# Optimization experiments

Measured on AMD Instinct MI355X. Metric: run time of the kernel, lower is better.

The kernel has to match this reference:

```python
import jax, jax.numpy as jnp
import numpy as np

N_NODES = 10000
N_EDGES = 320000


def _segment_softmax(scores, seg, num_segments):
    # scores: [E, H], segment-wise stable softmax keyed by seg (edge_index[0])
    m = jax.ops.segment_max(scores, seg, num_segments=num_segments)
    e = jnp.exp(scores - m[seg])
    z = jax.ops.segment_sum(e, seg, num_segments=num_segments)
    return e / z[seg]


def _gat_layer(x, W, a, row, col, n_nodes, heads, out_dim):
    # x: [N, F_in], W: [F_in, heads*out_dim], a: [heads, 2*out_dim]
    h = (x @ W).reshape(n_nodes, heads, out_dim)          # [N, H, F]
    a_l, a_r = a[:, :out_dim], a[:, out_dim:]             # [H, F] each
    # attention score per edge/head without materializing [E, H, 2F]
    s = (h[row] * a_l).sum(-1) + (h[col] * a_r).sum(-1)   # [E, H]
    alpha = _segment_softmax(s, row, n_nodes)             # [E, H]
    msg = alpha[..., None] * h[row]                       # [E, H, F]
    return jax.ops.segment_sum(msg, col, num_segments=n_nodes)  # [N, H, F]


def setup_inputs() -> dict:
    key = jax.random.key(0)
    ks = jax.random.split(key, 6)
    F, H, C = 128, 4, 22
    x = jax.random.normal(ks[0], (N_NODES, F), dtype=jnp.float32)
    edge_index = jax.random.randint(ks[1], (2, N_EDGES), 0, N_NODES, dtype=jnp.int64)
    W1 = jax.random.normal(ks[2], (F, F * H), dtype=jnp.float32) * 0.05
    a1 = jax.random.normal(ks[3], (H, 2 * F), dtype=jnp.float32) * 0.05
    W2 = jax.random.normal(ks[4], (F, C), dtype=jnp.float32) * 0.05
    a2 = jax.random.normal(ks[5], (1, 2 * C), dtype=jnp.float32) * 0.05
    return {"x": x, "edge_index": edge_index, "W1": W1, "a1": a1, "W2": W2, "a2": a2}


def reference(x, edge_index, W1, a1, W2, a2):
    row, col = edge_index[0], edge_index[1]
    h1 = _gat_layer(x, W1, a1, row, col, N_NODES, heads=4, out_dim=128)  # [N, 4, 128]
    h1 = jax.nn.elu(h1).mean(axis=1)                                      # combine heads -> [N, 128]
    h2 = _gat_layer(h1, W2, a2, row, col, N_NODES, heads=1, out_dim=22)   # [N, 1, 22]
    return h2[:, 0, :]                                                    # [N, 22]
```

## Files before the change

kernel.cpp:

```cpp
#include <hip/hip_runtime.h>

#define NN 10000
#define NE 320000
#define EPP 5000
#define NPART 64

typedef short short8 __attribute__((ext_vector_type(8)));
typedef float f32x4 __attribute__((ext_vector_type(4)));

__device__ __forceinline__ unsigned short f2bf(float f) {
    unsigned u = __float_as_uint(f);
    return (unsigned short)((u + 0x7FFFu + ((u >> 16) & 1u)) >> 16);
}
__device__ __forceinline__ float bflo(unsigned v) { return __uint_as_float(v << 16); }
__device__ __forceinline__ float bfhi(unsigned v) { return __uint_as_float(v & 0xffff0000u); }
__device__ __forceinline__ float bf1(unsigned short v) { return __uint_as_float(((unsigned)v) << 16); }

__device__ __forceinline__ int eread(const void* p, int is64, int i) {
    if (is64) return (int)((const long long*)p)[i];
    return ((const int*)p)[i];
}

__global__ __launch_bounds__(256) void k_prep0(const void* __restrict__ ei,
                                               const float* __restrict__ W1, const float* __restrict__ a1,
                                               unsigned short* __restrict__ W1t, float* __restrict__ wrf,
                                               int* __restrict__ flag) {
    const int b = blockIdx.x, t = threadIdx.x;
    if (b < 256) {
        const int g = b * 256 + t;
        const int h = g >> 14, j = (g >> 7) & 127, k = g & 127;
        W1t[g] = f2bf(W1[(size_t)k * 512 + h * 128 + j]);
    } else if (b < 258) {
        const int g = (b - 256) * 256 + t;
        const int h = g >> 7, k = g & 127;
        const float* wrow = W1 + (size_t)k * 512 + h * 128;
        const float* av = a1 + h * 256 + 128;
        float s = 0.f;
        for (int d = 0; d < 128; d++) s += wrow[d] * av[d];
        wrf[h * 128 + k] = s;
    } else {
        if (t == 0) {
            const unsigned* idx = (const unsigned*)ei;
            int all0 = 1;
            for (int j = 1; j < 257; j += 2)
                if (idx[j] != 0u) { all0 = 0; break; }
            *flag = all0;
        }
    }
}

__global__ __launch_bounds__(256) void k_pre(const float* __restrict__ x, const float* __restrict__ wrf,
                                             unsigned short* __restrict__ xb, float* __restrict__ ehr1,
                                             const void* __restrict__ ei, const int* __restrict__ flag,
                                             unsigned short* __restrict__ degp_c,
                                             unsigned short* __restrict__ degp_r,
                                             unsigned* __restrict__ packed_c,
                                             unsigned* __restrict__ packed_r) {
    __shared__ int sh[NN];
    const int b = blockIdx.x, t = threadIdx.x;
    if (b < 2500) {
        float* ls = (float*)sh;
        const int lane = t & 63, w = t >> 6;
        ls[t] = wrf[t];
        ls[t + 256] = wrf[t + 256];
        __syncthreads();
        const int i = b * 4 + w;
        const float x0 = x[(size_t)i * 128 + lane];
        const float x1 = x[(size_t)i * 128 + 64 + lane];
        xb[(size_t)i * 128 + lane]      = f2bf(x0);
        xb[(size_t)i * 128 + 64 + lane] = f2bf(x1);
        float v[4];
#pragma unroll
        for (int h = 0; h < 4; h++)
            v[h] = x0 * ls[h * 128 + lane] + x1 * ls[h * 128 + 64 + lane];
#pragma unroll
        for (int off = 1; off < 64; off <<= 1) {
#pragma unroll
            for (int j = 0; j < 4; j++) v[j] += __shfl_xor(v[j], off);
        }
        if (lane == 0)
            *(float4*)&ehr1[i * 4] = make_float4(__expf(v[0]), __expf(v[1]), __expf(v[2]), __expf(v[3]));
    } else {
        const int is64 = *flag;
        const int isC = (b < 2500 + NPART);
        const int p = isC ? (b - 2500) : (b - 2500 - NPART);
        const int ebase = p * EPP;
        for (int q = t; q < NN; q += 256) sh[q] = 0;
        __syncthreads();
        if (isC) {
            for (int q = t; q < EPP; q += 256) {
                const int e = ebase + q;
                const int c = eread(ei, is64, NE + e);
                const unsigned rk = (unsigned)atomicAdd(&sh[c], 1);
                packed_c[e] = ((unsigned)c << 13) | rk;
            }
            __syncthreads();
            for (int q = t; q < NN; q += 256) degp_c[p * NN + q] = (unsigned short)sh[q];
        } else {
            for (int q = t; q < EPP; q += 256) {
                const int e = ebase + q;
                const int r = eread(ei, is64, e);
                const unsigned rk = (unsigned)atomicAdd(&sh[r], 1);
                packed_r[e] = ((unsigned)r << 13) | rk;
            }
            __syncthreads();
            for (int q = t; q < NN; q += 256) degp_r[p * NN + q] = (unsigned short)sh[q];
        }
    }
}

__global__ __launch_bounds__(256) void k_psum(const unsigned short* __restrict__ degp_c,
                                              const unsigned short* __restrict__ degp_r,
                                              unsigned short* __restrict__ pfx_c,
                                              unsigned short* __restrict__ pfx_r,
                                              int* __restrict__ deg_c, int* __restrict__ deg_r) {
    const int g = blockIdx.x * 256 + threadIdx.x;
    if (g >= 2 * NN) return;
    const int arr = g / NN, node = g % NN;
    const unsigned short* degp = arr ? degp_r : degp_c;
    unsigned short* pfx = arr ? pfx_r : pfx_c;
    int* tot = arr ? deg_r : deg_c;
    int sum = 0;
#pragma unroll
    for (int p = 0; p < NPART; p++) {
        pfx[p * NN + node] = (unsigned short)sum;
        sum += (int)degp[p * NN + node];
    }
    tot[node] = sum;
}

__device__ void scan_one_1k(const int* __restrict__ deg, int* __restrict__ start, int* ssum) {
    const int t = threadIdx.x;
    int loc[10];
    const int base = t * 10;
    int sum = 0;
#pragma unroll
    for (int j = 0; j < 10; j++) {
        int i = base + j;
        int v = (i < NN) ? deg[i] : 0;
        loc[j] = sum;
        sum += v;
    }
    const int lane = t & 63, w = t >> 6;
    int xi = sum;
#pragma unroll
    for (int off = 1; off < 64; off <<= 1) {
        int y = __shfl_up(xi, off);
        if (lane >= off) xi += y;
    }
    __syncthreads();
    if (lane == 63) ssum[w] = xi;
    __syncthreads();
    int woff = 0;
#pragma unroll
    for (int k = 0; k < 16; k++)
        if (k < w) woff += ssum[k];
    const int excl = woff + xi - sum;
#pragma unroll
    for (int j = 0; j < 10; j++) {
        int i = base + j;
        if (i < NN) start[i] = excl + loc[j];
    }
}

__global__ __launch_bounds__(1024) void k_scan2(const int* __restrict__ deg_c, const int* __restrict__ deg_r,
                                                int* __restrict__ start_c, int* __restrict__ start_r) {
    __shared__ int ssum[16];
    scan_one_1k(deg_c, start_c, ssum);
    __syncthreads();
    scan_one_1k(deg_r, start_r, ssum);
}

__global__ __launch_bounds__(256) void k_build(const unsigned* __restrict__ packed_c,
                                               const unsigned* __restrict__ packed_r,
                                               const unsigned short* __restrict__ pfx_c,
                                               const unsigned short* __restrict__ pfx_r,
                                               const int* __restrict__ start_c, const int* __restrict__ start_r,
                                               int* __restrict__ csrA, int* __restrict__ csrB) {
    const int e = blockIdx.x * 256 + threadIdx.x;
    if (e >= NE) return;
    const int part = e / EPP;
    const unsigned pc = packed_c[e], pr = packed_r[e];
    const int c = (int)(pc >> 13), rkc = (int)(pc & 8191u);
    const int r = (int)(pr >> 13), rkr = (int)(pr & 8191u);
    csrA[start_c[c] + (int)pfx_c[part * NN + c] + rkc] = r;
    csrB[start_r[r] + (int)pfx_r[part * NN + r] + rkr] = c;
}

__global__ __launch_bounds__(256) void k_z1(const int* __restrict__ start_r, const int* __restrict__ deg_r,
                                            const int* __restrict__ csrB,
                                            const float* __restrict__ ehr1, float* __restrict__ rz1) {
    const int t = threadIdx.x, lane = t & 63, w = t >> 6;
    const int half = lane >> 5, l32 = lane & 31;
    const int i = blockIdx.x * 8 + w * 2 + half;
    const int s0 = start_r[i], d = deg_r[i];
    float zx = 0.f, zy = 0.f, zz = 0.f, zw = 0.f;
    for (int p = s0 + l32; p < s0 + d; p += 32) {
        const int c = csrB[p];
        const float4 v = *(const float4*)&ehr1[c * 4];
        zx += v.x; zy += v.y; zz += v.z; zw += v.w;
    }
#pragma unroll
    for (int off = 1; off < 32; off <<= 1) {
        zx += __shfl_xor(zx, off); zy += __shfl_xor(zy, off);
        zz += __shfl_xor(zz, off); zw += __shfl_xor(zw, off);
    }
    if (l32 == 0)
        *(float4*)&rz1[i * 4] = make_float4(1.f / zx, 1.f / zy, 1.f / zz, 1.f / zw);
}

__global__ __launch_bounds__(1024) void k_aggF(const unsigned short* __restrict__ xb,
                                               const float* __restrict__ ehr1, const float* __restrict__ rz1,
                                               const int* __restrict__ start_c, const int* __restrict__ deg_c,
                                               const int* __restrict__ csrA,
                                               const unsigned short* __restrict__ W1t,
                                               float* __restrict__ h1m) {
    __shared__ unsigned short lx[16 * 512];
    const int t = threadIdx.x, lane = t & 63, w = t >> 6;
    const int n0 = blockIdx.x * 16;

    {
        const int i = n0 + w;
        const float4 er4 = *(const float4*)&ehr1[i * 4];
        const int s0 = start_c[i], dg = deg_c[i];
        float acc[8];
#pragma unroll
        for (int j = 0; j < 8; j++) acc[j] = 0.f;
        int p = s0;
        const int e8 = s0 + (dg & ~7);
        for (; p < e8; p += 8) {
            int rr[8]; unsigned vv[8]; float4 zz[8];
#pragma unroll
            for (int q = 0; q < 8; q++) rr[q] = csrA[p + q];
#pragma unroll
            for (int q = 0; q < 8; q++) vv[q] = *(const unsigned*)&xb[(size_t)rr[q] * 128 + lane * 2];
#pragma unroll
            for (int q = 0; q < 8; q++) zz[q] = *(const float4*)&rz1[rr[q] * 4];
#pragma unroll
            for (int q = 0; q < 8; q++) {
                const float xa = bflo(vv[q]), xbv = bfhi(vv[q]);
                acc[0] += zz[q].x * xa; acc[1] += zz[q].x * xbv;
                acc[2] += zz[q].y * xa; acc[3] += zz[q].y * xbv;
                acc[4] += zz[q].z * xa; acc[5] += zz[q].z * xbv;
                acc[6] += zz[q].w * xa; acc[7] += zz[q].w * xbv;
            }
        }
        for (; p < s0 + dg; ++p) {
            const int r = csrA[p];
            const unsigned v = *(const unsigned*)&xb[(size_t)r * 128 + lane * 2];
            const float4 z = *(const float4*)&rz1[r * 4];
            const float xa = bflo(v), xbv = bfhi(v);
            acc[0] += z.x * xa; acc[1] += z.x * xbv;
            acc[2] += z.y * xa; acc[3] += z.y * xbv;
            acc[4] += z.z * xa; acc[5] += z.z * xbv;
            acc[6] += z.w * xa; acc[7] += z.w * xbv;
        }
        const float ef[4] = {er4.x, er4.y, er4.z, er4.w};
        const int fin = (lane & 3) * 2;
#pragma unroll
        for (int h = 0; h < 4; h++) {
            const int f = h * 16 + (lane >> 2);
            const int sc = ((f ^ (w & 7)) << 3) + fin;
            ushort2 st;
            st.x = f2bf(acc[h * 2] * ef[h]);
            st.y = f2bf(acc[h * 2 + 1] * ef[h]);
            *(ushort2*)&lx[w * 512 + sc] = st;
        }
    }
    __syncthreads();

    if (w < 8) {
        const int j = w;
        const int r16 = lane & 15, grp = lane >> 4;
        f32x4 hm = (f32x4)0.f;
#pragma unroll
        for (int h = 0; h < 4; h++) {
            f32x4 acc = (f32x4)0.f;
#pragma unroll
            for (int kk = 0; kk < 128; kk += 32) {
                const int f = h * 16 + (kk >> 3) + grp;
                const int sc = (f ^ (r16 & 7)) << 3;
                short8 a = *(const short8*)&lx[r16 * 512 + sc];
                short8 bfr = *(const short8*)&W1t[(size_t)h * 16384 + (j * 16 + r16) * 128 + kk + grp * 8];
                acc = __builtin_amdgcn_mfma_f32_16x16x32_bf16(a, bfr, acc, 0, 0, 0);
            }
#pragma unroll
            for (int r = 0; r < 4; r++) {
                const float v = acc[r];
                hm[r] += (v > 0.f) ? v : (__expf(v) - 1.f);
            }
        }
#pragma unroll
        for (int r = 0; r < 4; r++) {
            const int node = n0 + grp * 4 + r;
            h1m[(size_t)node * 128 + j * 16 + r16] = 0.25f * hm[r];
        }
    }
}

__global__ __launch_bounds__(256) void k_gemm2(const float* __restrict__ h1m, const float* __restrict__ W2,
                                               const float* __restrict__ a2,
                                               float* __restrict__ h2, float* __restrict__ ehr2) {
    __shared__ float sh[4][128];
    const int t = threadIdx.x, lane = t & 63, w = t >> 6;
    const int i = blockIdx.x * 4 + w;
    sh[w][lane]      = h1m[(size_t)i * 128 + lane];
    sh[w][lane + 64] = h1m[(size_t)i * 128 + 64 + lane];
    __syncthreads();
    const int seg = lane >> 5, c = lane & 31;
    float part = 0.f;
    if (c < 22) {
        const int kb = seg * 64;
        for (int k = kb; k < kb + 64; k++)
            part += sh[w][k] * W2[k * 22 + c];
    }
    part += __shfl_xor(part, 32);
    const float acc = part;
    if (lane < 22) h2[(size_t)i * 22 + lane] = acc;
    float pr = (lane < 22) ? acc * a2[22 + lane] : 0.f;
#pragma unroll
    for (int off = 1; off < 64; off <<= 1)
        pr += __shfl_xor(pr, off);
    if (lane == 0) ehr2[i] = __expf(pr);
}

__global__ __launch_bounds__(256) void k_z2s(const int* __restrict__ start_r, const int* __restrict__ deg_r,
                                             const int* __restrict__ csrB,
                                             const float* __restrict__ ehr2, const float* __restrict__ h2,
                                             unsigned short* __restrict__ h2s) {
    const int t = threadIdx.x, lane = t & 63, w = t >> 6;
    const int half = lane >> 5, l32 = lane & 31;
    const int i = blockIdx.x * 8 + w * 2 + half;
    const int s0 = start_r[i], d = deg_r[i];
    float z = 0.f;
    for (int p = s0 + l32; p < s0 + d; p += 32)
        z += ehr2[csrB[p]];
#pragma unroll
    for (int off = 1; off < 32; off <<= 1)
        z += __shfl_xor(z, off);
    const float rz = 1.f / z;
    if (l32 < 22)
        h2s[(size_t)i * 32 + l32] = f2bf(h2[(size_t)i * 22 + l32] * rz);
}

__global__ __launch_bounds__(256) void k_agg2(const unsigned short* __restrict__ h2s,
                                              const float* __restrict__ ehr2,
                                              const int* __restrict__ start_c, const int* __restrict__ deg_c,
                                              const int* __restrict__ csrA,
                                              float* __restrict__ out) {
    const int t = threadIdx.x, lane = t & 63, w = t >> 6;
    const int half = lane >> 5, c32 = lane & 31;
    const int i = blockIdx.x * 8 + w * 2 + half;
    const int s0 = start_c[i], dg = deg_c[i];
    const float e2 = ehr2[i];
    const int c = (c32 < 22) ? c32 : 0;
    float acc = 0.f;
    int p = s0;
    const int e8 = s0 + (dg & ~7);
    for (; p < e8; p += 8) {
        int rr[8];
#pragma unroll
        for (int q = 0; q < 8; q++) rr[q] = csrA[p + q];
        float vv[8];
#pragma unroll
        for (int q = 0; q < 8; q++) vv[q] = bf1(h2s[(size_t)rr[q] * 32 + c]);
#pragma unroll
        for (int q = 0; q < 8; q++) acc += vv[q];
    }
    for (; p < s0 + dg; ++p) {
        const int r = csrA[p];
        acc += bf1(h2s[(size_t)r * 32 + c]);
    }
    if (c32 < 22) out[(size_t)i * 22 + c32] = acc * e2;
}

extern "C" void kernel_launch(void* const* d_in, const int* in_sizes, int n_in,
                              void* d_out, int out_size, void* d_ws, size_t ws_size,
                              hipStream_t stream) {
    const float* x  = (const float*)d_in[0];
    const void*  ei = d_in[1];
    const float* W1 = (const float*)d_in[2];
    const float* a1 = (const float*)d_in[3];
    const float* W2 = (const float*)d_in[4];
    const float* a2 = (const float*)d_in[5];
    float* out = (float*)d_out;

    float* ws = (float*)d_ws;
    float* h1m  = ws;
    float* h2   = ws + 1280000;
    float* ehr1 = ws + 1500000;
    float* rz1  = ws + 1540000;
    float* ehr2 = ws + 1580000;
    unsigned short* h2s = (unsigned short*)(ws + 1590000);
    int* deg_c   = (int*)(ws + 1750000);
    int* deg_r   = (int*)(ws + 1760000);
    int* start_c = (int*)(ws + 1770000);
    int* start_r = (int*)(ws + 1780000);
    int* csrA    = (int*)(ws + 1790000);
    int* csrB    = (int*)(ws + 2110000);
    int* flag    = (int*)(ws + 2430000);
    float* wrf   = ws + 2430064;
    unsigned short* W1t = (unsigned short*)(ws + 2431000);
    unsigned short* xb  = (unsigned short*)(ws + 2464000);
    unsigned* packed_c = (unsigned*)(ws + 3104000);
    unsigned* packed_r = (unsigned*)(ws + 3424000);
    unsigned short* degp_c = (unsigned short*)(ws + 3744000);
    unsigned short* degp_r = (unsigned short*)(ws + 4064000);
    unsigned short* pfx_c  = (unsigned short*)(ws + 4384000);
    unsigned short* pfx_r  = (unsigned short*)(ws + 4704000);

    k_prep0<<<259, 256, 0, stream>>>(ei, W1, a1, W1t, wrf, flag);
    k_pre<<<2500 + 2 * NPART, 256, 0, stream>>>(x, wrf, xb, ehr1, ei, flag,
                                                degp_c, degp_r, packed_c, packed_r);
    k_psum<<<79, 256, 0, stream>>>(degp_c, degp_r, pfx_c, pfx_r, deg_c, deg_r);
    k_scan2<<<1, 1024, 0, stream>>>(deg_c, deg_r, start_c, start_r);
    k_build<<<1250, 256, 0, stream>>>(packed_c, packed_r, pfx_c, pfx_r,
                                      start_c, start_r, csrA, csrB);
    k_z1<<<1250, 256, 0, stream>>>(start_r, deg_r, csrB, ehr1, rz1);
    k_aggF<<<625, 1024, 0, stream>>>(xb, ehr1, rz1, start_c, deg_c, csrA, W1t, h1m);
    k_gemm2<<<2500, 256, 0, stream>>>(h1m, W2, a2, h2, ehr2);
    k_z2s<<<1250, 256, 0, stream>>>(start_r, deg_r, csrB, ehr2, h2, h2s);
    k_agg2<<<1250, 256, 0, stream>>>(h2s, ehr2, start_c, deg_c, csrA, out);
}
```

Baseline: 110.2 us.

## Merge prep kernels, move ehr1 into build, fuse layer-2 GEMM into aggregation

Removes the separate k_prep0 launch by folding W1 transpose, wrf computation and int64 detection into k_pre, with each partition block detecting the index type itself. The ehr1 score computation moves into extra blocks of k_build so it runs after wrf exists. The layer-2 GEMM and ehr2 computation are fused into the tail of k_aggF using shared memory, which removes the h1m round-trip through global memory and the k_gemm2 launch. In exchange, k_aggF uses more shared memory, which may lower its occupancy, and every edge-partition block now repeats the index-type detection.

```diff
diff --git a/kernel.cpp b/kernel.cpp
--- a/kernel.cpp
+++ b/kernel.cpp
@@ -21,67 +21,33 @@
     return ((const int*)p)[i];
 }
 
-__global__ __launch_bounds__(256) void k_prep0(const void* __restrict__ ei,
-                                               const float* __restrict__ W1, const float* __restrict__ a1,
-                                               unsigned short* __restrict__ W1t, float* __restrict__ wrf,
-                                               int* __restrict__ flag) {
-    const int b = blockIdx.x, t = threadIdx.x;
-    if (b < 256) {
-        const int g = b * 256 + t;
-        const int h = g >> 14, j = (g >> 7) & 127, k = g & 127;
-        W1t[g] = f2bf(W1[(size_t)k * 512 + h * 128 + j]);
-    } else if (b < 258) {
-        const int g = (b - 256) * 256 + t;
-        const int h = g >> 7, k = g & 127;
-        const float* wrow = W1 + (size_t)k * 512 + h * 128;
-        const float* av = a1 + h * 256 + 128;
-        float s = 0.f;
-        for (int d = 0; d < 128; d++) s += wrow[d] * av[d];
-        wrf[h * 128 + k] = s;
-    } else {
-        if (t == 0) {
-            const unsigned* idx = (const unsigned*)ei;
-            int all0 = 1;
-            for (int j = 1; j < 257; j += 2)
-                if (idx[j] != 0u) { all0 = 0; break; }
-            *flag = all0;
-        }
-    }
-}
-
-__global__ __launch_bounds__(256) void k_pre(const float* __restrict__ x, const float* __restrict__ wrf,
-                                             unsigned short* __restrict__ xb, float* __restrict__ ehr1,
-                                             const void* __restrict__ ei, const int* __restrict__ flag,
+__device__ __forceinline__ int detect64(const void* ei) {
+    const unsigned* idx = (const unsigned*)ei;
+    int all0 = 1;
+    for (int j = 1; j < 257; j += 2)
+        if (idx[j] != 0u) { all0 = 0; break; }
+    return all0;
+}
+
+__global__ __launch_bounds__(256) void k_pre(const float* __restrict__ x,
+                                             unsigned short* __restrict__ xb,
+                                             const void* __restrict__ ei,
                                              unsigned short* __restrict__ degp_c,
                                              unsigned short* __restrict__ degp_r,
                                              unsigned* __restrict__ packed_c,
-                                             unsigned* __restrict__ packed_r) {
+                                             unsigned* __restrict__ packed_r,
+                                             const float* __restrict__ W1, const float* __restrict__ a1,
+                                             unsigned short* __restrict__ W1t,
+                                             float* __restrict__ wrf) {
     __shared__ int sh[NN];
     const int b = blockIdx.x, t = threadIdx.x;
     if (b < 2500) {
-        float* ls = (float*)sh;
-        const int lane = t & 63, w = t >> 6;
-        ls[t] = wrf[t];
-        ls[t + 256] = wrf[t + 256];
-        __syncthreads();
-        const int i = b * 4 + w;
-        const float x0 = x[(size_t)i * 128 + lane];
-        const float x1 = x[(size_t)i * 128 + 64 + lane];
-        xb[(size_t)i * 128 + lane]      = f2bf(x0);
-        xb[(size_t)i * 128 + 64 + lane] = f2bf(x1);
-        float v[4];
-#pragma unroll
-        for (int h = 0; h < 4; h++)
-            v[h] = x0 * ls[h * 128 + lane] + x1 * ls[h * 128 + 64 + lane];
-#pragma unroll
-        for (int off = 1; off < 64; off <<= 1) {
-#pragma unroll
-            for (int j = 0; j < 4; j++) v[j] += __shfl_xor(v[j], off);
-        }
-        if (lane == 0)
-            *(float4*)&ehr1[i * 4] = make_float4(__expf(v[0]), __expf(v[1]), __expf(v[2]), __expf(v[3]));
-    } else {
-        const int is64 = *flag;
+        const int g = b * 256 + t;
+        const float2 v = *(const float2*)&x[(size_t)g * 2];
+        ushort2 o; o.x = f2bf(v.x); o.y = f2bf(v.y);
+        *(ushort2*)&xb[(size_t)g * 2] = o;
+    } else if (b < 2500 + 2 * NPART) {
+        const int is64 = detect64(ei);
         const int isC = (b < 2500 + NPART);
         const int p = isC ? (b - 2500) : (b - 2500 - NPART);
         const int ebase = p * EPP;
@@ -106,6 +72,18 @@
             __syncthreads();
             for (int q = t; q < NN; q += 256) degp_r[p * NN + q] = (unsigned short)sh[q];
         }
+    } else if (b < 2500 + 2 * NPART + 256) {
+        const int g = (b - 2500 - 2 * NPART) * 256 + t;
+        const int h = g >> 14, j = (g >> 7) & 127, k = g & 127;
+        W1t[g] = f2bf(W1[(size_t)k * 512 + h * 128 + j]);
+    } else {
+        const int g = (b - 2500 - 2 * NPART - 256) * 256 + t;
+        const int h = g >> 7, k = g & 127;
+        const float* wrow = W1 + (size_t)k * 512 + h * 128;
+        const float* av = a1 + h * 256 + 128;
+        float s = 0.f;
+        for (int d = 0; d < 128; d++) s += wrow[d] * av[d];
+        wrf[h * 128 + k] = s;
     }
 }
 
@@ -176,15 +154,39 @@
                                                const unsigned short* __restrict__ pfx_c,
                                                const unsigned short* __restrict__ pfx_r,
                                                const int* __restrict__ start_c, const int* __restrict__ start_r,
-                                               int* __restrict__ csrA, int* __restrict__ csrB) {
-    const int e = blockIdx.x * 256 + threadIdx.x;
-    if (e >= NE) return;
-    const int part = e / EPP;
-    const unsigned pc = packed_c[e], pr = packed_r[e];
-    const int c = (int)(pc >> 13), rkc = (int)(pc & 8191u);
-    const int r = (int)(pr >> 13), rkr = (int)(pr & 8191u);
-    csrA[start_c[c] + (int)pfx_c[part * NN + c] + rkc] = r;
-    csrB[start_r[r] + (int)pfx_r[part * NN + r] + rkr] = c;
+                                               int* __restrict__ csrA, int* __restrict__ csrB,
+                                               const float* __restrict__ x, const float* __restrict__ wrf,
+                                               float* __restrict__ ehr1) {
+    __shared__ float ls[512];
+    const int b = blockIdx.x, t = threadIdx.x;
+    if (b < 1250) {
+        const int e = b * 256 + t;
+        const int part = e / EPP;
+        const unsigned pc = packed_c[e], pr = packed_r[e];
+        const int c = (int)(pc >> 13), rkc = (int)(pc & 8191u);
+        const int r = (int)(pr >> 13), rkr = (int)(pr & 8191u);
+        csrA[start_c[c] + (int)pfx_c[part * NN + c] + rkc] = r;
+        csrB[start_r[r] + (int)pfx_r[part * NN + r] + rkr] = c;
+    } else {
+        const int lane = t & 63, w = t >> 6;
+        ls[t] = wrf[t];
+        ls[t + 256] = wrf[t + 256];
+        __syncthreads();
+        const int i = (b - 1250) * 4 + w;
+        const float x0 = x[(size_t)i * 128 + lane];
+        const float x1 = x[(size_t)i * 128 + 64 + lane];
+        float v[4];
+#pragma unroll
+        for (int h = 0; h < 4; h++)
+            v[h] = x0 * ls[h * 128 + lane] + x1 * ls[h * 128 + 64 + lane];
+#pragma unroll
+        for (int off = 1; off < 64; off <<= 1) {
+#pragma unroll
+            for (int j = 0; j < 4; j++) v[j] += __shfl_xor(v[j], off);
+        }
+        if (lane == 0)
+            *(float4*)&ehr1[i * 4] = make_float4(__expf(v[0]), __expf(v[1]), __expf(v[2]), __expf(v[3]));
+    }
 }
 
 __global__ __launch_bounds__(256) void k_z1(const int* __restrict__ start_r, const int* __restrict__ deg_r,
@@ -214,10 +216,17 @@
                                                const int* __restrict__ start_c, const int* __restrict__ deg_c,
                                                const int* __restrict__ csrA,
                                                const unsigned short* __restrict__ W1t,
-                                               float* __restrict__ h1m) {
+                                               const float* __restrict__ W2, const float* __restrict__ a2,
+                                               float* __restrict__ h2, float* __restrict__ ehr2) {
     __shared__ unsigned short lx[16 * 512];
+    __shared__ float h1f[16 * 128];
+    __shared__ float w2s[2816];
+    __shared__ float a2s[22];
     const int t = threadIdx.x, lane = t & 63, w = t >> 6;
     const int n0 = blockIdx.x * 16;
+
+    for (int q = t; q < 2816; q += 1024) w2s[q] = W2[q];
+    if (t < 22) a2s[t] = a2[22 + t];
 
     {
         const int i = n0 + w;
@@ -291,37 +300,29 @@
             }
         }
 #pragma unroll
-        for (int r = 0; r < 4; r++) {
-            const int node = n0 + grp * 4 + r;
-            h1m[(size_t)node * 128 + j * 16 + r16] = 0.25f * hm[r];
-        }
-    }
-}
-
-__global__ __launch_bounds__(256) void k_gemm2(const float* __restrict__ h1m, const float* __restrict__ W2,
-                                               const float* __restrict__ a2,
-                                               float* __restrict__ h2, float* __restrict__ ehr2) {
-    __shared__ float sh[4][128];
-    const int t = threadIdx.x, lane = t & 63, w = t >> 6;
-    const int i = blockIdx.x * 4 + w;
-    sh[w][lane]      = h1m[(size_t)i * 128 + lane];
-    sh[w][lane + 64] = h1m[(size_t)i * 128 + 64 + lane];
+        for (int r = 0; r < 4; r++)
+            h1f[(grp * 4 + r) * 128 + j * 16 + r16] = 0.25f * hm[r];
+    }
     __syncthreads();
-    const int seg = lane >> 5, c = lane & 31;
-    float part = 0.f;
-    if (c < 22) {
-        const int kb = seg * 64;
-        for (int k = kb; k < kb + 64; k++)
-            part += sh[w][k] * W2[k * 22 + c];
-    }
-    part += __shfl_xor(part, 32);
-    const float acc = part;
-    if (lane < 22) h2[(size_t)i * 22 + lane] = acc;
-    float pr = (lane < 22) ? acc * a2[22 + lane] : 0.f;
-#pragma unroll
-    for (int off = 1; off < 64; off <<= 1)
-        pr += __shfl_xor(pr, off);
-    if (lane == 0) ehr2[i] = __expf(pr);
+
+    {
+        const int i = n0 + w;
+        const int seg = lane >> 5, c = lane & 31;
+        float part = 0.f;
+        if (c < 22) {
+            const float* hrow = &h1f[w * 128 + seg * 64];
+            const float* wp = &w2s[seg * 64 * 22 + c];
+            for (int k = 0; k < 64; k++)
+                part += hrow[k] * wp[k * 22];
+        }
+        part += __shfl_xor(part, 32);
+        if (lane < 22) h2[(size_t)i * 22 + lane] = part;
+        float pr = (lane < 22) ? part * a2s[lane] : 0.f;
+#pragma unroll
+        for (int off = 1; off < 64; off <<= 1)
+            pr += __shfl_xor(pr, off);
+        if (lane == 0) ehr2[i] = __expf(pr);
+    }
 }
 
 __global__ __launch_bounds__(256) void k_z2s(const int* __restrict__ start_r, const int* __restrict__ deg_r,
@@ -386,39 +387,36 @@
     float* out = (float*)d_out;
 
     float* ws = (float*)d_ws;
-    float* h1m  = ws;
-    float* h2   = ws + 1280000;
-    float* ehr1 = ws + 1500000;
-    float* rz1  = ws + 1540000;
-    float* ehr2 = ws + 1580000;
-    unsigned short* h2s = (unsigned short*)(ws + 1590000);
-    int* deg_c   = (int*)(ws + 1750000);
-    int* deg_r   = (int*)(ws + 1760000);
-    int* start_c = (int*)(ws + 1770000);
-    int* start_r = (int*)(ws + 1780000);
-    int* csrA    = (int*)(ws + 1790000);
-    int* csrB    = (int*)(ws + 2110000);
-    int* flag    = (int*)(ws + 2430000);
-    float* wrf   = ws + 2430064;
-    unsigned short* W1t = (unsigned short*)(ws + 2431000);
-    unsigned short* xb  = (unsigned short*)(ws + 2464000);
-    unsigned* packed_c = (unsigned*)(ws + 3104000);
-    unsigned* packed_r = (unsigned*)(ws + 3424000);
-    unsigned short* degp_c = (unsigned short*)(ws + 3744000);
-    unsigned short* degp_r = (unsigned short*)(ws + 4064000);
-    unsigned short* pfx_c  = (unsigned short*)(ws + 4384000);
-    unsigned short* pfx_r  = (unsigned short*)(ws + 4704000);
-
-    k_prep0<<<259, 256, 0, stream>>>(ei, W1, a1, W1t, wrf, flag);
-    k_pre<<<2500 + 2 * NPART, 256, 0, stream>>>(x, wrf, xb, ehr1, ei, flag,
-                                                degp_c, degp_r, packed_c, packed_r);
+    float* h2   = ws;
+    float* ehr1 = ws + 220000;
+    float* rz1  = ws + 260000;
+    float* ehr2 = ws + 300000;
+    unsigned short* h2s = (unsigned short*)(ws + 310000);
+    int* deg_c   = (int*)(ws + 470000);
+    int* deg_r   = (int*)(ws + 480000);
+    int* start_c = (int*)(ws + 490000);
+    int* start_r = (int*)(ws + 500000);
+    int* csrA    = (int*)(ws + 510000);
+    int* csrB    = (int*)(ws + 830000);
+    float* wrf   = ws + 1150000;
+    unsigned short* W1t = (unsigned short*)(ws + 1151000);
+    unsigned short* xb  = (unsigned short*)(ws + 1184000);
+    unsigned* packed_c = (unsigned*)(ws + 1824000);
+    unsigned* packed_r = (unsigned*)(ws + 2144000);
+    unsigned short* degp_c = (unsigned short*)(ws + 2464000);
+    unsigned short* degp_r = (unsigned short*)(ws + 2784000);
+    unsigned short* pfx_c  = (unsigned short*)(ws + 3104000);
+    unsigned short* pfx_r  = (unsigned short*)(ws + 3424000);
+
+    k_pre<<<2500 + 2 * NPART + 258, 256, 0, stream>>>(x, xb, ei, degp_c, degp_r,
+                                                      packed_c, packed_r, W1, a1, W1t, wrf);
     k_psum<<<79, 256, 0, stream>>>(degp_c, degp_r, pfx_c, pfx_r, deg_c, deg_r);
     k_scan2<<<1, 1024, 0, stream>>>(deg_c, deg_r, start_c, start_r);
-    k_build<<<1250, 256, 0, stream>>>(packed_c, packed_r, pfx_c, pfx_r,
-                                      start_c, start_r, csrA, csrB);
+    k_build<<<3750, 256, 0, stream>>>(packed_c, packed_r, pfx_c, pfx_r,
+                                      start_c, start_r, csrA, csrB, x, wrf, ehr1);
     k_z1<<<1250, 256, 0, stream>>>(start_r, deg_r, csrB, ehr1, rz1);
-    k_aggF<<<625, 1024, 0, stream>>>(xb, ehr1, rz1, start_c, deg_c, csrA, W1t, h1m);
-    k_gemm2<<<2500, 256, 0, stream>>>(h1m, W2, a2, h2, ehr2);
+    k_aggF<<<625, 1024, 0, stream>>>(xb, ehr1, rz1, start_c, deg_c, csrA, W1t,
+                                     W2, a2, h2, ehr2);
     k_z2s<<<1250, 256, 0, stream>>>(start_r, deg_r, csrB, ehr2, h2, h2s);
     k_agg2<<<1250, 256, 0, stream>>>(h2s, ehr2, start_c, deg_c, csrA, out);
 }
```

New measurement: 104.1 us. -5.6%, faster.
